# Kernel tuning notes

Measured on AMD Instinct MI355X. Metric: run time of the kernel, lower is better.

Reference implementation:

```python
import jax, jax.numpy as jnp
import numpy as np

DIM = 768      # model dim
NH = 12        # num heads
WS = 32        # window/input size (H = W = WS)
B = 8          # batch


def _relative_position_index(ws):
    # Mirrors the torch buffer construction.
    coords = np.stack(np.meshgrid(np.arange(ws), np.arange(ws), indexing='ij'))  # [2, ws, ws]
    cf = coords.reshape(2, -1)                                # [2, N]
    rel = cf[:, :, None] - cf[:, None, :]                     # [2, N, N]
    rel = rel.transpose(1, 2, 0).astype(np.int64)             # [N, N, 2]
    rel[..., 0] += ws - 1
    rel[..., 1] += ws - 1
    rel[..., 0] *= 2 * ws - 1
    return rel.sum(-1)                                        # [N, N]


def setup_inputs() -> dict:
    key = jax.random.key(0)
    ks = jax.random.split(key, 5)
    std = 0.02
    x = jax.random.normal(ks[0], (B, WS, WS, DIM), jnp.float32)
    qkv_w = jax.random.normal(ks[1], (3 * DIM, DIM), jnp.float32) * std
    q_bias = jnp.zeros((DIM,), jnp.float32)
    v_bias = jnp.zeros((DIM,), jnp.float32)
    proj_w = jax.random.normal(ks[2], (DIM, DIM), jnp.float32) * std
    proj_b = jnp.zeros((DIM,), jnp.float32)
    num_rel = (2 * WS - 1) * (2 * WS - 1) + 3
    rel_table = jax.random.normal(ks[3], (num_rel, NH), jnp.float32) * std
    rel_index = jnp.asarray(_relative_position_index(WS), jnp.int32)
    return {
        'x': x, 'qkv_w': qkv_w, 'q_bias': q_bias, 'v_bias': v_bias,
        'proj_w': proj_w, 'proj_b': proj_b, 'rel_table': rel_table,
        'rel_index': rel_index,
    }


def reference(x, qkv_w, q_bias, v_bias, proj_w, proj_b, rel_table, rel_index):
    Bb, H, W, C = x.shape
    N = H * W
    hd = C // NH
    scale = hd ** (-0.5)
    # qkv bias: [q_bias, zeros(k), v_bias]
    qkv_b = jnp.concatenate([q_bias, jnp.zeros_like(v_bias), v_bias])
    qkv = x.reshape(Bb, N, C) @ qkv_w.T + qkv_b                # [B, N, 3C]
    qkv = qkv.reshape(Bb, N, 3, NH, hd).transpose(2, 0, 3, 1, 4)  # [3, B, nh, N, hd]
    q, k, v = qkv[0] * scale, qkv[1], qkv[2]
    attn = jnp.einsum('bhqd,bhkd->bhqk', q, k)                 # [B, nh, N, N]
    bias = rel_table[rel_index.reshape(-1)].reshape(N, N, NH)  # [N, N, nh]
    bias = bias.transpose(2, 0, 1)                             # [nh, N, N]
    attn = jax.nn.softmax(attn + bias[None], axis=-1)
    out = jnp.einsum('bhqk,bhkd->bhqd', attn, v)               # [B, nh, N, hd]
    out = out.transpose(0, 2, 1, 3).reshape(Bb, H, W, C)
    return out @ proj_w.T + proj_b
```

## Files before the change

### kernel.cpp

```cpp
#include <hip/hip_runtime.h>
#include <cstdint>
#include <cstddef>

#define DIMC 768
#define NHH  12
#define NSEQ 1024
#define HD   64

#define SX  6291456
#define SW1 1769472
#define SW2 589824

#define RELN 3969
#define RELP 4032

typedef _Float16 f16x8 __attribute__((ext_vector_type(8)));
typedef _Float16 f16x4 __attribute__((ext_vector_type(4)));
typedef float    f32x4 __attribute__((ext_vector_type(4)));
typedef float    f32x16 __attribute__((ext_vector_type(16)));
typedef float    f32x4u __attribute__((ext_vector_type(4), aligned(4)));

__device__ inline void gld16(const _Float16* g, _Float16* l) {
  __builtin_amdgcn_global_load_lds(
      (const __attribute__((address_space(1))) void*)g,
      (__attribute__((address_space(3))) void*)l, 16, 0, 0);
}

__global__ __launch_bounds__(256) void cast_f16(
    const float* __restrict__ x, const float* __restrict__ w1,
    const float* __restrict__ w2, _Float16* __restrict__ dst) {
  const long long t = (long long)blockIdx.x * 256 + threadIdx.x;
  const long long i = t * 8;
  const float* src; long long off;
  if (i < SX) { src = x; off = i; }
  else if (i < SX + SW1) { src = w1; off = i - SX; }
  else { src = w2; off = i - (SX + SW1); }
  const float4 a = *(const float4*)(src + off);
  const float4 b = *(const float4*)(src + off + 4);
  f16x8 o;
  o[0] = (_Float16)a.x; o[1] = (_Float16)a.y; o[2] = (_Float16)a.z; o[3] = (_Float16)a.w;
  o[4] = (_Float16)b.x; o[5] = (_Float16)b.y; o[6] = (_Float16)b.z; o[7] = (_Float16)b.w;
  *(f16x8*)(dst + i) = o;
}

template <int EPI>
__global__ __launch_bounds__(256) void gemm_mfma(
    const _Float16* __restrict__ A, const _Float16* __restrict__ W,
    const float* __restrict__ b0, const float* __restrict__ b1,
    float* __restrict__ outF, _Float16* __restrict__ oq,
    _Float16* __restrict__ ok, _Float16* __restrict__ ovt) {
  __shared__ _Float16 Alds[128 * 32];
  __shared__ _Float16 Blds[128 * 32];

  const int tid = threadIdx.x;
  const int w = tid >> 6, lane = tid & 63, quad = lane >> 4, l16 = lane & 15;
  const int m0 = (blockIdx.x & 63) << 7;
  const int o0 = (blockIdx.x >> 6) << 7;
  const int wr = (w >> 1) * 64, wc = (w & 1) * 64;

  f32x4 acc[4][4];
#pragma unroll
  for (int i = 0; i < 4; i++)
#pragma unroll
    for (int j = 0; j < 4; j++) acc[i][j] = (f32x4){0.f, 0.f, 0.f, 0.f};

  const int c0 = tid, c1 = 256 + tid;
  const int r0 = c0 >> 2, cb0 = (c0 & 3) * 8;
  const int r1 = c1 >> 2, cb1 = (c1 & 3) * 8;
  const _Float16* Ap0 = A + (size_t)(m0 + r0) * DIMC + cb0;
  const _Float16* Ap1 = A + (size_t)(m0 + r1) * DIMC + cb1;
  const _Float16* Wp0 = W + (size_t)(o0 + r0) * DIMC + cb0;
  const _Float16* Wp1 = W + (size_t)(o0 + r1) * DIMC + cb1;

  for (int k0 = 0; k0 < DIMC; k0 += 32) {
    __syncthreads();
    gld16(Ap0 + k0, &Alds[c0 * 8]);
    gld16(Ap1 + k0, &Alds[c1 * 8]);
    gld16(Wp0 + k0, &Blds[c0 * 8]);
    gld16(Wp1 + k0, &Blds[c1 * 8]);
    __syncthreads();

    f16x8 a[4], b[4];
#pragma unroll
    for (int i = 0; i < 4; i++)
      a[i] = *(const f16x8*)&Alds[(wr + i * 16 + l16) * 32 + quad * 8];
#pragma unroll
    for (int j = 0; j < 4; j++)
      b[j] = *(const f16x8*)&Blds[(wc + j * 16 + l16) * 32 + quad * 8];
#pragma unroll
    for (int i = 0; i < 4; i++)
#pragma unroll
      for (int j = 0; j < 4; j++)
        acc[i][j] = __builtin_amdgcn_mfma_f32_16x16x32_f16(a[i], b[j], acc[i][j], 0, 0, 0);
  }

  if constexpr (EPI == 0) {
#pragma unroll
    for (int j = 0; j < 4; j++) {
      const int o = o0 + wc + j * 16 + l16;
      const int part = o / DIMC;
      const int cc = o - part * DIMC;
      const int hh = cc >> 6, d = cc & 63;
      const float badd = (part == 0) ? b0[cc] : (part == 2 ? b1[cc] : 0.f);
      if (part == 2) {
#pragma unroll
        for (int i = 0; i < 4; i++) {
          const int mb = m0 + wr + i * 16 + quad * 4;
          const int bb = mb >> 10, n0 = mb & 1023;
          f16x4 vv;
#pragma unroll
          for (int r = 0; r < 4; r++) vv[r] = (_Float16)(acc[i][j][r] + badd);
          *(f16x4*)(ovt + (((size_t)(bb * NHH + hh)) * HD + d) * NSEQ + n0) = vv;
        }
      } else {
        _Float16* dst = (part == 0) ? oq : ok;
#pragma unroll
        for (int i = 0; i < 4; i++) {
#pragma unroll
          for (int r = 0; r < 4; r++) {
            const int m = m0 + wr + i * 16 + quad * 4 + r;
            const int bb = m >> 10, n = m & 1023;
            float v = acc[i][j][r];
            if (part == 0) v = (v + badd) * 0.125f;
            dst[(((size_t)(bb * NHH + hh)) * NSEQ + n) * HD + d] = (_Float16)v;
          }
        }
      }
    }
  } else {
#pragma unroll
    for (int j = 0; j < 4; j++) {
      const int o = o0 + wc + j * 16 + l16;
      const float bo = b0[o];
#pragma unroll
      for (int i = 0; i < 4; i++) {
#pragma unroll
        for (int r = 0; r < 4; r++) {
          const int m = m0 + wr + i * 16 + quad * 4 + r;
          outF[(size_t)m * DIMC + o] = acc[i][j][r] + bo;
        }
      }
    }
  }
}

__global__ __launch_bounds__(256) void relt_pre(const float* __restrict__ rel_table,
                                                float* __restrict__ relT) {
  const int g = blockIdx.x * 256 + threadIdx.x;
  if (g >= NHH * RELN) return;
  const int h = g / RELN, idx = g - h * RELN;
  relT[h * RELP + idx] = rel_table[idx * NHH + h];
}

__global__ __launch_bounds__(256, 3) void flash_mfma(
    const _Float16* __restrict__ Qg, const _Float16* __restrict__ Kg,
    const _Float16* __restrict__ Vtg, const float* __restrict__ relT,
    _Float16* __restrict__ AO) {
  const int nblk = blockIdx.x;
  const int bhl = nblk % 96;
  const int qt = nblk / 96;
  const int head = bhl >> 3, b = bhl & 7;
  const int bh = b * NHH + head;
  const int tid = threadIdx.x, w = tid >> 6, lane = tid & 63;
  const int ql = lane & 31;
  const int hf = lane >> 5;

  __shared__ _Float16 Klds[128 * 64];
  __shared__ _Float16 Vlds[64 * 128];

  const int qglob = qt * 128 + w * 32 + ql;
  const _Float16* Qrow = Qg + ((size_t)bh * NSEQ + qglob) * HD + hf * 8;
  f16x8 bq[4];
#pragma unroll
  for (int s = 0; s < 4; s++) bq[s] = *(const f16x8*)(Qrow + s * 16);

  f32x16 O0 = {}, O1 = {};
  float psum = 0.f;

  const _Float16* Kbase = Kg + (size_t)bh * NSEQ * HD;
  const _Float16* Vtbase = Vtg + (size_t)bh * HD * NSEQ;

  const float* relTh = relT + (size_t)head * RELP;
  const int qy = qt * 4 + w;
  const int idxb = ql + 31 - 4 * hf;

  const int vrow0 = ql, vrow1 = 32 + ql;
  const int vkey0 = (vrow0 ^ (vrow0 >> 3)) & 7;
  const int vkey1 = (vrow1 ^ (vrow1 >> 3)) & 7;

  int ksrc[4], vsrc[4];
#pragma unroll
  for (int c4 = 0; c4 < 4; c4++) {
    const int c = tid + c4 * 256;
    const int kr = c >> 3, kcL = c & 7;
    const int kkey = (kr ^ (kr >> 3)) & 7;
    ksrc[c4] = kr * HD + (kcL ^ kkey) * 8;
    const int vr = c >> 4, vcL = c & 15;
    const int vkey = (vr ^ (vr >> 3)) & 7;
    vsrc[c4] = vr * NSEQ + (vcL ^ vkey) * 8;
  }

  for (int kt = 0; kt < 8; kt++) {
    __syncthreads();
#pragma unroll
    for (int c4 = 0; c4 < 4; c4++) {
      const int c = tid + c4 * 256;
      gld16(Kbase + (size_t)kt * 128 * HD + ksrc[c4], &Klds[c * 8]);
      gld16(Vtbase + kt * 128 + vsrc[c4], &Vlds[c * 8]);
    }
    __syncthreads();

#pragma unroll
    for (int t = 0; t < 4; t++) {
      const int arow = t * 32 + ql;
      const int akey = (arow ^ (arow >> 3)) & 7;
      f32x16 S = {};
      __builtin_amdgcn_s_setprio(1);
#pragma unroll
      for (int s = 0; s < 4; s++) {
        const f16x8 ak = *(const f16x8*)&Klds[((arow << 3) | ((s * 2 + hf) ^ akey)) * 8];
        S = __builtin_amdgcn_mfma_f32_32x32x16_f16(ak, bq[s], S, 0, 0, 0);
      }
      __builtin_amdgcn_s_setprio(0);

      const float* rowb = relTh + (qy - (kt * 4 + t) + 31) * 63 + idxb;
      unsigned int dw[8];
#pragma unroll
      for (int g = 0; g < 4; g++) {
        const f32x4u bv = *(const f32x4u*)(rowb - 8 * g - 3);
        const float p0 = __expf(S[4 * g + 0] + bv[3]);
        const float p1 = __expf(S[4 * g + 1] + bv[2]);
        const float p2 = __expf(S[4 * g + 2] + bv[1]);
        const float p3 = __expf(S[4 * g + 3] + bv[0]);
        psum += (p0 + p1) + (p2 + p3);
        union { f16x4 h; unsigned int u[2]; } cv;
        cv.h[0] = (_Float16)p0; cv.h[1] = (_Float16)p1;
        cv.h[2] = (_Float16)p2; cv.h[3] = (_Float16)p3;
        dw[2 * g] = cv.u[0]; dw[2 * g + 1] = cv.u[1];
      }

      __builtin_amdgcn_s_setprio(1);
#pragma unroll
      for (int s = 0; s < 2; s++) {
        const unsigned int x0 = hf ? dw[4 * s + 0] : dw[4 * s + 2];
        const unsigned int x1 = hf ? dw[4 * s + 1] : dw[4 * s + 3];
        const unsigned int y0 = (unsigned int)__shfl_xor((int)x0, 32, 64);
        const unsigned int y1 = (unsigned int)__shfl_xor((int)x1, 32, 64);
        union { unsigned int u[4]; f16x8 v; } bp;
        if (hf == 0) {
          bp.u[0] = dw[4 * s + 0]; bp.u[1] = dw[4 * s + 1];
          bp.u[2] = y0;            bp.u[3] = y1;
        } else {
          bp.u[0] = y0;            bp.u[1] = y1;
          bp.u[2] = dw[4 * s + 2]; bp.u[3] = dw[4 * s + 3];
        }
        const int kchunk = t * 4 + s * 2 + hf;
        const f16x8 av0 = *(const f16x8*)&Vlds[((vrow0 << 4) | (kchunk ^ vkey0)) * 8];
        O0 = __builtin_amdgcn_mfma_f32_32x32x16_f16(av0, bp.v, O0, 0, 0, 0);
        const f16x8 av1 = *(const f16x8*)&Vlds[((vrow1 << 4) | (kchunk ^ vkey1)) * 8];
        O1 = __builtin_amdgcn_mfma_f32_32x32x16_f16(av1, bp.v, O1, 0, 0, 0);
      }
      __builtin_amdgcn_s_setprio(0);
    }
  }

  psum += __shfl_xor(psum, 32, 64);
  const float inv = 1.f / psum;
  _Float16* aoRow = AO + ((size_t)(b * NSEQ + qglob)) * DIMC + head * HD;
#pragma unroll
  for (int g = 0; g < 4; g++) {
    f16x4 o0, o1;
#pragma unroll
    for (int j = 0; j < 4; j++) {
      o0[j] = (_Float16)(O0[4 * g + j] * inv);
      o1[j] = (_Float16)(O1[4 * g + j] * inv);
    }
    const int d0 = 8 * g + 4 * hf;
    *(f16x4*)(aoRow + d0) = o0;
    *(f16x4*)(aoRow + 32 + d0) = o1;
  }
}

extern "C" void kernel_launch(void* const* d_in, const int* in_sizes, int n_in,
                              void* d_out, int out_size, void* d_ws, size_t ws_size,
                              hipStream_t stream) {
  const float* x        = (const float*)d_in[0];
  const float* qkv_w    = (const float*)d_in[1];
  const float* q_bias   = (const float*)d_in[2];
  const float* v_bias   = (const float*)d_in[3];
  const float* proj_w   = (const float*)d_in[4];
  const float* proj_b   = (const float*)d_in[5];
  const float* rel_tab  = (const float*)d_in[6];
  float* out = (float*)d_out;

  const size_t NTOK = (size_t)8 * NHH * NSEQ * HD;
  _Float16* Xb     = (_Float16*)d_ws;
  _Float16* Wqkvb  = Xb + SX;
  _Float16* Wprojb = Wqkvb + SW1;
  _Float16* Qb     = Wprojb + SW2;
  _Float16* Kb     = Qb + NTOK;
  _Float16* Vt     = Kb + NTOK;
  float*    relT   = (float*)(Vt + NTOK);
  _Float16* AOb    = Xb;

  cast_f16<<<dim3((SX + SW1 + SW2) / 2048), 256, 0, stream>>>(x, qkv_w, proj_w, Xb);

  relt_pre<<<dim3((NHH * RELN + 255) / 256), 256, 0, stream>>>(rel_tab, relT);

  gemm_mfma<0><<<dim3(64 * 18), 256, 0, stream>>>(
      Xb, Wqkvb, q_bias, v_bias, nullptr, Qb, Kb, Vt);

  flash_mfma<<<dim3(768), 256, 0, stream>>>(Qb, Kb, Vt, relT, AOb);

  gemm_mfma<1><<<dim3(64 * 6), 256, 0, stream>>>(
      AOb, Wprojb, proj_b, nullptr, out, nullptr, nullptr, nullptr);
}
```

Before: 222.8 us.

## Double-buffer K/V tiles and stage relative bias through LDS in flash kernel

The flash attention loop now works on 64-key tiles with two LDS buffers, prefetching the next tile's K, V and relative-position bias rows while the current tile is computed. This drops one barrier per iteration. Bias values are read from LDS instead of unaligned global loads. The trade-off is smaller tiles, twice as many iterations, extra LDS for the bias buffer, and a single barrier guarding buffer reuse, which could create a race if the async loads are not waited on correctly.

Measured after the change: 211.0 us. 1.06x faster.

```diff
diff --git a/kernel.cpp b/kernel.cpp
--- a/kernel.cpp
+++ b/kernel.cpp
@@ -18,9 +18,8 @@
 typedef _Float16 f16x4 __attribute__((ext_vector_type(4)));
 typedef float    f32x4 __attribute__((ext_vector_type(4)));
 typedef float    f32x16 __attribute__((ext_vector_type(16)));
-typedef float    f32x4u __attribute__((ext_vector_type(4), aligned(4)));
-
-__device__ inline void gld16(const _Float16* g, _Float16* l) {
+
+__device__ inline void gld16(const void* g, void* l) {
   __builtin_amdgcn_global_load_lds(
       (const __attribute__((address_space(1))) void*)g,
       (__attribute__((address_space(3))) void*)l, 16, 0, 0);
@@ -165,8 +164,9 @@
   const int ql = lane & 31;
   const int hf = lane >> 5;
 
-  __shared__ _Float16 Klds[128 * 64];
-  __shared__ _Float16 Vlds[64 * 128];
+  __shared__ _Float16 Klds[2][64 * 64];
+  __shared__ _Float16 Vlds[2][64 * 64];
+  __shared__ __attribute__((aligned(16))) float BiasLds[2][320];
 
   const int qglob = qt * 128 + w * 32 + ql;
   const _Float16* Qrow = Qg + ((size_t)bh * NSEQ + qglob) * HD + hf * 8;
@@ -181,57 +181,70 @@
   const _Float16* Vtbase = Vtg + (size_t)bh * HD * NSEQ;
 
   const float* relTh = relT + (size_t)head * RELP;
-  const int qy = qt * 4 + w;
   const int idxb = ql + 31 - 4 * hf;
 
   const int vrow0 = ql, vrow1 = 32 + ql;
   const int vkey0 = (vrow0 ^ (vrow0 >> 3)) & 7;
   const int vkey1 = (vrow1 ^ (vrow1 >> 3)) & 7;
 
-  int ksrc[4], vsrc[4];
-#pragma unroll
-  for (int c4 = 0; c4 < 4; c4++) {
-    const int c = tid + c4 * 256;
-    const int kr = c >> 3, kcL = c & 7;
-    const int kkey = (kr ^ (kr >> 3)) & 7;
-    ksrc[c4] = kr * HD + (kcL ^ kkey) * 8;
-    const int vr = c >> 4, vcL = c & 15;
-    const int vkey = (vr ^ (vr >> 3)) & 7;
-    vsrc[c4] = vr * NSEQ + (vcL ^ vkey) * 8;
-  }
-
-  for (int kt = 0; kt < 8; kt++) {
+  int ks0, ks1, vs0, vs1;
+  {
+    int c = tid;
+    int r = c >> 3, cc = c & 7, key = (r ^ (r >> 3)) & 7;
+    ks0 = r * HD + (cc ^ key) * 8;
+    vs0 = r * NSEQ + (cc ^ key) * 8;
+    c = tid + 256;
+    r = c >> 3; cc = c & 7; key = (r ^ (r >> 3)) & 7;
+    ks1 = r * HD + (cc ^ key) * 8;
+    vs1 = r * NSEQ + (cc ^ key) * 8;
+  }
+
+  auto stage = [&](int s, int bsel) {
+    const _Float16* Ks = Kbase + (size_t)s * 64 * HD;
+    const _Float16* Vs = Vtbase + s * 64;
+    gld16(Ks + ks0, &Klds[bsel][tid * 8]);
+    gld16(Ks + ks1, &Klds[bsel][(tid + 256) * 8]);
+    gld16(Vs + vs0, &Vlds[bsel][tid * 8]);
+    gld16(Vs + vs1, &Vlds[bsel][(tid + 256) * 8]);
+    if (tid < 79) {
+      const int dyLo = qt * 4 + 30 - 2 * s;
+      gld16(relTh + dyLo * 63 + tid * 4, &BiasLds[bsel][tid * 4]);
+    }
+  };
+
+  stage(0, 0);
+
+  int cur = 0;
+#pragma unroll 2
+  for (int s = 0; s < 16; s++) {
     __syncthreads();
-#pragma unroll
-    for (int c4 = 0; c4 < 4; c4++) {
-      const int c = tid + c4 * 256;
-      gld16(Kbase + (size_t)kt * 128 * HD + ksrc[c4], &Klds[c * 8]);
-      gld16(Vtbase + kt * 128 + vsrc[c4], &Vlds[c * 8]);
-    }
-    __syncthreads();
-
-#pragma unroll
-    for (int t = 0; t < 4; t++) {
+    if (s + 1 < 16) stage(s + 1, cur ^ 1);
+
+#pragma unroll
+    for (int t = 0; t < 2; t++) {
       const int arow = t * 32 + ql;
       const int akey = (arow ^ (arow >> 3)) & 7;
       f32x16 S = {};
       __builtin_amdgcn_s_setprio(1);
 #pragma unroll
-      for (int s = 0; s < 4; s++) {
-        const f16x8 ak = *(const f16x8*)&Klds[((arow << 3) | ((s * 2 + hf) ^ akey)) * 8];
-        S = __builtin_amdgcn_mfma_f32_32x32x16_f16(ak, bq[s], S, 0, 0, 0);
+      for (int ss = 0; ss < 4; ss++) {
+        const f16x8 ak = *(const f16x8*)&Klds[cur][((arow << 3) | ((ss * 2 + hf) ^ akey)) * 8];
+        S = __builtin_amdgcn_mfma_f32_32x32x16_f16(ak, bq[ss], S, 0, 0, 0);
       }
       __builtin_amdgcn_s_setprio(0);
 
-      const float* rowb = relTh + (qy - (kt * 4 + t) + 31) * 63 + idxb;
+      const float* lb = &BiasLds[cur][(w + 1 - t) * 63 + idxb];
       unsigned int dw[8];
 #pragma unroll
       for (int g = 0; g < 4; g++) {
-        const f32x4u bv = *(const f32x4u*)(rowb - 8 * g - 3);
-        const float p0 = __expf(S[4 * g + 0] + bv[3]);
-        const float p1 = __expf(S[4 * g + 1] + bv[2]);
-        const float p2 = __expf(S[4 * g + 2] + bv[1]);
-        const float p3 = __expf(S[4 * g + 3] + bv[0]);
+        const float b0 = lb[-8 * g - 0];
+        const float b1 = lb[-8 * g - 1];
+        const float b2 = lb[-8 * g - 2];
+        const float b3 = lb[-8 * g - 3];
+        const float p0 = __expf(S[4 * g + 0] + b0);
+        const float p1 = __expf(S[4 * g + 1] + b1);
+        const float p2 = __expf(S[4 * g + 2] + b2);
+        const float p3 = __expf(S[4 * g + 3] + b3);
         psum += (p0 + p1) + (p2 + p3);
         union { f16x4 h; unsigned int u[2]; } cv;
         cv.h[0] = (_Float16)p0; cv.h[1] = (_Float16)p1;
@@ -241,27 +254,28 @@
 
       __builtin_amdgcn_s_setprio(1);
 #pragma unroll
-      for (int s = 0; s < 2; s++) {
-        const unsigned int x0 = hf ? dw[4 * s + 0] : dw[4 * s + 2];
-        const unsigned int x1 = hf ? dw[4 * s + 1] : dw[4 * s + 3];
+      for (int s2 = 0; s2 < 2; s2++) {
+        const unsigned int x0 = hf ? dw[4 * s2 + 0] : dw[4 * s2 + 2];
+        const unsigned int x1 = hf ? dw[4 * s2 + 1] : dw[4 * s2 + 3];
         const unsigned int y0 = (unsigned int)__shfl_xor((int)x0, 32, 64);
         const unsigned int y1 = (unsigned int)__shfl_xor((int)x1, 32, 64);
         union { unsigned int u[4]; f16x8 v; } bp;
         if (hf == 0) {
-          bp.u[0] = dw[4 * s + 0]; bp.u[1] = dw[4 * s + 1];
-          bp.u[2] = y0;            bp.u[3] = y1;
+          bp.u[0] = dw[4 * s2 + 0]; bp.u[1] = dw[4 * s2 + 1];
+          bp.u[2] = y0;             bp.u[3] = y1;
         } else {
-          bp.u[0] = y0;            bp.u[1] = y1;
-          bp.u[2] = dw[4 * s + 2]; bp.u[3] = dw[4 * s + 3];
+          bp.u[0] = y0;             bp.u[1] = y1;
+          bp.u[2] = dw[4 * s2 + 2]; bp.u[3] = dw[4 * s2 + 3];
         }
-        const int kchunk = t * 4 + s * 2 + hf;
-        const f16x8 av0 = *(const f16x8*)&Vlds[((vrow0 << 4) | (kchunk ^ vkey0)) * 8];
+        const int kchunk = t * 4 + s2 * 2 + hf;
+        const f16x8 av0 = *(const f16x8*)&Vlds[cur][((vrow0 << 3) | (kchunk ^ vkey0)) * 8];
         O0 = __builtin_amdgcn_mfma_f32_32x32x16_f16(av0, bp.v, O0, 0, 0, 0);
-        const f16x8 av1 = *(const f16x8*)&Vlds[((vrow1 << 4) | (kchunk ^ vkey1)) * 8];
+        const f16x8 av1 = *(const f16x8*)&Vlds[cur][((vrow1 << 3) | (kchunk ^ vkey1)) * 8];
         O1 = __builtin_amdgcn_mfma_f32_32x32x16_f16(av1, bp.v, O1, 0, 0, 0);
       }
       __builtin_amdgcn_s_setprio(0);
     }
+    cur ^= 1;
   }
 
   psum += __shfl_xor(psum, 32, 64);
```
